# Performance work log

Hardware: AMD Instinct MI355X
Metric: run time of the kernel (lower is better)

## Reference

```python
import jax, jax.numpy as jnp
import numpy as np

EPS = 1e-8      # module eps for attention renorm
LN_EPS = 1e-5   # torch LayerNorm default


def _lin(x, w, b):
    return x @ w + b


def _ln(x, g, b):
    m = jnp.mean(x, -1, keepdims=True)
    v = jnp.var(x, -1, keepdims=True)
    return (x - m) * jax.lax.rsqrt(v + LN_EPS) * g + b


def setup_inputs() -> dict:
    key = jax.random.key(0)
    it = iter(jax.random.split(key, 48))
    B, N, IC, EC, D, S = 8, 32768, 3, 63, 128, 8
    wf = lambda i, o: jax.random.normal(next(it), (i, o), jnp.float32) / np.sqrt(i)
    bf = lambda o: jax.random.normal(next(it), (o,), jnp.float32) * 0.02
    return {
        'inputs': jax.random.normal(next(it), (B, N, IC), jnp.float32),
        'embed_pts': jax.random.normal(next(it), (B, N, EC), jnp.float32),
        'slots_mu': jax.random.normal(next(it), (1, 1, D), jnp.float32),
        'slots_sigma': jax.random.normal(next(it), (1, 1, D), jnp.float32),
        'w0': wf(IC, 64), 'b0': bf(64),
        'w1': wf(64, 32), 'b1': bf(32),
        'w2': wf(32, 32), 'b2': bf(32),
        'w3': wf(32, 32), 'b3': bf(32),
        'w4': wf(32, 32), 'b4': bf(32),
        'w5': wf(32, 32), 'b5': bf(32),
        'w7': wf(IC + EC + 32, D), 'b7': bf(D),
        'wq': wf(D, D), 'bq': bf(D),
        'wk': wf(D, D), 'bk': bf(D),
        'wv': wf(D, D), 'bv': bf(D),
        'ln_in_g': jnp.ones((D,), jnp.float32), 'ln_in_b': jnp.zeros((D,), jnp.float32),
        'ln_sl_g': jnp.ones((D,), jnp.float32), 'ln_sl_b': jnp.zeros((D,), jnp.float32),
        'ln_ff_g': jnp.ones((D,), jnp.float32), 'ln_ff_b': jnp.zeros((D,), jnp.float32),
        'gru_wih': jax.random.normal(next(it), (3 * D, D), jnp.float32) / np.sqrt(D),
        'gru_whh': jax.random.normal(next(it), (3 * D, D), jnp.float32) / np.sqrt(D),
        'gru_bih': bf(3 * D), 'gru_bhh': bf(3 * D),
        'mlp1_w': wf(D, D), 'mlp1_b': bf(D),
        'mlp2_w': wf(D, D), 'mlp2_b': bf(D),
        'num_slots': S,
    }


def reference(inputs, embed_pts, slots_mu, slots_sigma, w0, b0, w1, b1, w2, b2, w3, b3, w4, b4, w5, b5, w7, b7, wq, bq, wk, bk, wv, bv, ln_in_g, ln_in_b, ln_sl_g, ln_sl_b, ln_ff_g, ln_ff_b, gru_wih, gru_whh, gru_bih, gru_bhh, mlp1_w, mlp1_b, mlp2_w, mlp2_b, num_slots):
    # dense stack (no nonlinearities in the original)
    x = inputs
    for w, b in ((w0, b0), (w1, b1), (w2, b2), (w3, b3), (w4, b4), (w5, b5)):
        x = _lin(x, w, b)
    h = _lin(jnp.concatenate([inputs, embed_pts, x], -1), w7, b7)  # [B,N,D]
    B, N, D = h.shape
    scale = D ** -0.5

    # slot init: torch.normal(mean(mu).data, std(sigma).data) over broadcast tensors
    mu = jnp.broadcast_to(slots_mu, (B, num_slots, D))
    sg = jnp.broadcast_to(slots_sigma, (B, num_slots, D))
    mean = jax.lax.stop_gradient(jnp.mean(mu))
    std = jax.lax.stop_gradient(jnp.std(sg, ddof=1))  # torch.std is unbiased
    slots = mean + std * jax.random.normal(jax.random.key(42), (B, num_slots, D), jnp.float32)

    h = _ln(h, ln_in_g, ln_in_b)
    k = _lin(h, wk, bk)
    v = _lin(h, wv, bv)

    for _ in range(3):  # iters
        slots_prev = slots
        q = _lin(_ln(slots, ln_sl_g, ln_sl_b), wq, bq)            # [B,S,D]
        dots = jnp.einsum('bid,bjd->bij', q, k) * scale           # [B,S,N]
        attn = jax.nn.softmax(dots, axis=1) + EPS                 # softmax over slots
        attn = attn / jnp.sum(attn, -1, keepdims=True)            # renorm over inputs
        updates = jnp.einsum('bjd,bij->bid', v, attn)             # [B,S,D]
        # GRUCell (torch semantics)
        xg = updates.reshape(-1, D)
        hp = slots_prev.reshape(-1, D)
        gi = xg @ gru_wih.T + gru_bih                             # [B*S,3D]
        gh = hp @ gru_whh.T + gru_bhh
        ir, iz, inn = jnp.split(gi, 3, axis=-1)
        hr, hz, hn = jnp.split(gh, 3, axis=-1)
        r = jax.nn.sigmoid(ir + hr)
        z = jax.nn.sigmoid(iz + hz)
        n = jnp.tanh(inn + r * hn)
        slots = ((1.0 - z) * n + z * hp).reshape(B, num_slots, D)
        # residual MLP (two linears, no activation, as in source)
        m = _lin(_lin(_ln(slots, ln_ff_g, ln_ff_b), mlp1_w, mlp1_b), mlp2_w, mlp2_b)
        slots = slots + m
    return slots.reshape(B, num_slots * D)
```

## Files before the change

### kernel.cpp

```cpp
#include <hip/hip_runtime.h>


#define B_  8
#define N_  32768
#define NB_ (B_ * N_)
#define D_  128
#define S_  8

typedef unsigned int u32;
typedef unsigned short u16;
typedef __attribute__((ext_vector_type(8))) short bf16x8;
typedef __attribute__((ext_vector_type(4))) float f32x4;

__device__ inline u32 bfr1(float x) {
    u32 u = __float_as_uint(x);
    return (u + 0x7FFFu + ((u >> 16) & 1u)) >> 16;
}
__device__ inline u32 bfpack2(u32 lo, u32 hi) { return lo | (hi << 16); }

__device__ inline void threefry42(u32 c0, u32 c1, u32& o0, u32& o1) {
    const u32 k0 = 0u, k1 = 42u, k2 = 0x1BD11BDAu ^ 0u ^ 42u;
    const u32 ks[3] = {k0, k1, k2};
    u32 x0 = c0 + k0, x1 = c1 + k1;
    const int rA[4] = {13, 15, 26, 6}, rB[4] = {17, 29, 16, 24};
#pragma unroll
    for (int i = 0; i < 5; i++) {
#pragma unroll
        for (int k = 0; k < 4; k++) {
            int r = (i & 1) ? rB[k] : rA[k];
            x0 += x1;
            x1 = (x1 << r) | (x1 >> (32 - r));
            x1 ^= x0;
        }
        x0 += ks[(i + 1) % 3];
        x1 += ks[(i + 2) % 3] + (u32)(i + 1);
    }
    o0 = x0; o1 = x1;
}

__device__ inline float bits_to_normal(u32 b) {
    float f = __uint_as_float((b >> 9) | 0x3f800000u) - 1.0f;
    const float lo = -0.99999994f;
    float r = fmaxf(lo, f * 1.99999994f + lo);
    float w = -log1pf(-r * r);
    float p;
    if (w < 5.0f) {
        w -= 2.5f;
        p = 2.81022636e-08f;
        p = fmaf(p, w, 3.43273939e-07f);
        p = fmaf(p, w, -3.5233877e-06f);
        p = fmaf(p, w, -4.39150654e-06f);
        p = fmaf(p, w, 0.00021858087f);
        p = fmaf(p, w, -0.00125372503f);
        p = fmaf(p, w, -0.00417768164f);
        p = fmaf(p, w, 0.246640727f);
        p = fmaf(p, w, 1.50140941f);
    } else {
        w = sqrtf(w) - 3.0f;
        p = -0.000200214257f;
        p = fmaf(p, w, 0.000100950558f);
        p = fmaf(p, w, 0.00134934322f);
        p = fmaf(p, w, -0.00367342844f);
        p = fmaf(p, w, 0.00573950773f);
        p = fmaf(p, w, -0.0076224613f);
        p = fmaf(p, w, 0.00943887047f);
        p = fmaf(p, w, 1.00167406f);
        p = fmaf(p, w, 2.83297682f);
    }
    return 1.41421356f * (p * r);
}

__device__ inline float block128_sum(float v, float* red) {
#pragma unroll
    for (int o = 32; o; o >>= 1) v += __shfl_down(v, o);
    __syncthreads();
    if ((threadIdx.x & 63) == 0) red[threadIdx.x >> 6] = v;
    __syncthreads();
    return red[0] + red[1];
}

__device__ void emit_q(float x, int bs,
                       const float* lnsg, const float* lnsb,
                       const float* wq, const float* bq,
                       const float* wkT, const float* bk,
                       float* qt, float* qc,
                       float* shA, float* red) {
    int t = threadIdx.x;
    float m = block128_sum(x, red) * (1.0f / 128.0f);
    float e = x - m;
    float var = block128_sum(e * e, red) * (1.0f / 128.0f);
    float inv = rsqrtf(var + 1e-5f);
    __syncthreads();
    shA[t] = fmaf(e * inv, lnsg[t], lnsb[t]);
    __syncthreads();
    float q = bq[t];
#pragma unroll 4
    for (int i = 0; i < 128; i++) q = fmaf(shA[i], wq[i * 128 + t], q);
    __syncthreads();
    shA[t] = q;
    __syncthreads();
    float a2 = 0.f;
#pragma unroll 4
    for (int j = 0; j < 128; j++) a2 = fmaf(wkT[j * 128 + t], shA[j], a2);
    const float scale = 0.08838834764831845f;
    qt[bs * 128 + t] = a2 * scale;
    float pr = block128_sum(shA[t] * bk[t], red);
    if (t == 0) qc[bs] = pr * scale;
}


__global__ __launch_bounds__(256) void k0_transpose(
    const float* __restrict__ wih, const float* __restrict__ whh,
    const float* __restrict__ wk,
    float* __restrict__ wihT, float* __restrict__ whhT, float* __restrict__ wkT) {
    int idx = blockIdx.x * 256 + threadIdx.x;
    if (idx < 49152) {
        int d = idx / 384, g = idx % 384;
        wihT[idx] = wih[g * 128 + d];
    } else if (idx < 98304) {
        int o = idx - 49152;
        int d = o / 384, g = o % 384;
        whhT[o] = whh[g * 128 + d];
    } else if (idx < 114688) {
        int o = idx - 98304;
        int j = o >> 7, tcol = o & 127;
        wkT[o] = wk[tcol * 128 + j];
    }
}


__global__ __launch_bounds__(256) void k1_setup(
    const float* __restrict__ w0, const float* __restrict__ b0,
    const float* __restrict__ w1, const float* __restrict__ b1,
    const float* __restrict__ w2, const float* __restrict__ b2,
    const float* __restrict__ w3, const float* __restrict__ b3,
    const float* __restrict__ w4, const float* __restrict__ b4,
    const float* __restrict__ w5, const float* __restrict__ b5,
    const float* __restrict__ w7, const float* __restrict__ b7,
    const float* __restrict__ mu, const float* __restrict__ sg,
    float* __restrict__ Wh, float* __restrict__ bh, float* __restrict__ slots,
    u16* __restrict__ whiT) {
    __shared__ float A[192], Bt[96], bb[64], bb2[32];
    __shared__ float stats[2];
    int t = threadIdx.x;
    for (int i = t; i < 192; i += 256) A[i] = w0[i];
    for (int i = t; i < 64; i += 256) bb[i] = b0[i];
    __syncthreads();
    const float* wl[5] = {w1, w2, w3, w4, w5};
    const float* bl[5] = {b1, b2, b3, b4, b5};
    int kin = 64;
    for (int l = 0; l < 5; l++) {
        const float* w = wl[l];
        const float* bias = bl[l];
        if (t < 96) {
            int i = t / 32, j = t % 32;
            float acc = 0.f;
            for (int k = 0; k < kin; k++) acc += A[i * kin + k] * w[k * 32 + j];
            Bt[i * 32 + j] = acc;
        } else if (t < 128) {
            int j = t - 96;
            float acc = bias[j];
            for (int k = 0; k < kin; k++) acc += bb[k] * w[k * 32 + j];
            bb2[j] = acc;
        }
        __syncthreads();
        if (t < 96) A[t] = Bt[t];
        if (t < 32) bb[t] = bb2[t];
        __syncthreads();
        kin = 32;
    }
    for (int idx = t; idx < 66 * 128; idx += 256) {
        int i = idx >> 7, j = idx & 127;
        float acc = w7[idx];
        if (i < 3) {
            for (int k = 0; k < 32; k++) acc += A[i * 32 + k] * w7[(66 + k) * 128 + j];
        }
        Wh[idx] = acc;
    }
    for (int j = t; j < 128; j += 256) {
        float acc = b7[j];
        for (int k = 0; k < 32; k++) acc += bb[k] * w7[(66 + k) * 128 + j];
        bh[j] = acc;
    }
    if (t == 0) {
        float s1 = 0.f, s2 = 0.f;
        for (int d = 0; d < 128; d++) { s1 += mu[d]; s2 += sg[d]; }
        float mmu = s1 / 128.f, msg = s2 / 128.f;
        float ss = 0.f;
        for (int d = 0; d < 128; d++) { float e = sg[d] - msg; ss += e * e; }
        stats[0] = mmu;
        stats[1] = sqrtf(64.f * ss / 8191.f);
    }
    __syncthreads();
    for (int idx = t; idx < 128 * 96; idx += 256) {
        int col = idx / 96, k = idx - col * 96;
        float v = (k < 66) ? Wh[k * 128 + col] : 0.f;
        whiT[idx] = (u16)bfr1(v);
    }
    float mean = stats[0], sd = stats[1];
    for (int p = t; p < 8192; p += 256) {
        u32 o0, o1;
        threefry42(0u, (u32)p, o0, o1);
        slots[p] = fmaf(sd, bits_to_normal(o0 ^ o1), mean);
    }
}


__global__ __launch_bounds__(256) void k2_hln(
    const float* __restrict__ inputs, const float* __restrict__ embed,
    const u16* __restrict__ whiT, const float* __restrict__ bh,
    const float* __restrict__ g, const float* __restrict__ bbias,
    u16* __restrict__ hlnb) {
    __shared__ __align__(16) char smem[34816];
    __shared__ float bhl[128], gl[128], bl[128];
    int t = threadIdx.x;
    u16* ebuf = (u16*)smem;
    size_t rbase = (size_t)blockIdx.x * 128;
    for (int idx = t; idx < 384; idx += 256)
        ebuf[(idx / 3) * 104 + (idx % 3)] = (u16)bfr1(inputs[rbase * 3 + idx]);
    for (int idx = t; idx < 128 * 63; idx += 256) {
        int r = idx / 63, i = idx - r * 63;
        ebuf[r * 104 + 3 + i] = (u16)bfr1(embed[rbase * 63 + idx]);
    }
    for (int idx = t; idx < 128 * 30; idx += 256) {
        int r = idx / 30, i = idx - r * 30;
        ebuf[r * 104 + 66 + i] = 0;
    }
    if (t < 128) { bhl[t] = bh[t]; gl[t] = g[t]; bl[t] = bbias[t]; }
    __syncthreads();

    int w = t >> 6, l = t & 63;
    int c16 = l & 15, g4 = l >> 4;
    int wr0 = w * 32;
    float bhc[8], gc[8], bc[8];
#pragma unroll
    for (int nt = 0; nt < 8; nt++) {
        bhc[nt] = bhl[nt * 16 + c16];
        gc[nt] = gl[nt * 16 + c16];
        bc[nt] = bl[nt * 16 + c16];
    }
    f32x4 acc[2][8];
#pragma unroll
    for (int mi = 0; mi < 2; mi++)
#pragma unroll
        for (int nt = 0; nt < 8; nt++)
            acc[mi][nt] = (f32x4){bhc[nt], bhc[nt], bhc[nt], bhc[nt]};

#pragma unroll
    for (int kc = 0; kc < 3; kc++) {
        bf16x8 a0 = *(const bf16x8*)&ebuf[(wr0 + c16) * 104 + kc * 32 + g4 * 8];
        bf16x8 a1 = *(const bf16x8*)&ebuf[(wr0 + 16 + c16) * 104 + kc * 32 + g4 * 8];
#pragma unroll
        for (int nt = 0; nt < 8; nt++) {
            uint4 bw = *(const uint4*)(whiT + (size_t)(nt * 16 + c16) * 96 + kc * 32 + g4 * 8);
            bf16x8 bf = *(bf16x8*)&bw;
            acc[0][nt] = __builtin_amdgcn_mfma_f32_16x16x32_bf16(a0, bf, acc[0][nt], 0, 0, 0);
            acc[1][nt] = __builtin_amdgcn_mfma_f32_16x16x32_bf16(a1, bf, acc[1][nt], 0, 0, 0);
        }
    }

    __syncthreads();
    u16* T = (u16*)smem;
#pragma unroll
    for (int mi = 0; mi < 2; mi++) {
#pragma unroll
        for (int i = 0; i < 4; i++) {
            float s = 0.f;
#pragma unroll
            for (int nt = 0; nt < 8; nt++) s += acc[mi][nt][i];
            s += __shfl_xor(s, 1); s += __shfl_xor(s, 2);
            s += __shfl_xor(s, 4); s += __shfl_xor(s, 8);
            float m = s * (1.0f / 128.0f);
            float v = 0.f;
#pragma unroll
            for (int nt = 0; nt < 8; nt++) { float d = acc[mi][nt][i] - m; v = fmaf(d, d, v); }
            v += __shfl_xor(v, 1); v += __shfl_xor(v, 2);
            v += __shfl_xor(v, 4); v += __shfl_xor(v, 8);
            float inv = rsqrtf(v * (1.0f / 128.0f) + 1e-5f);
            int row = wr0 + mi * 16 + g4 * 4 + i;
#pragma unroll
            for (int nt = 0; nt < 8; nt++) {
                float val = fmaf((acc[mi][nt][i] - m) * inv, gc[nt], bc[nt]);
                T[row * 136 + nt * 16 + c16] = (u16)bfr1(val);
            }
        }
    }
    __syncthreads();
    {
        int r = t >> 1, hf = t & 1;
        const u16* Tr = T + r * 136 + hf * 64;
        u16* dst = hlnb + (rbase + r) * 128 + hf * 64;
#pragma unroll
        for (int j = 0; j < 8; j++) {
            uint4 v = *(const uint4*)(Tr + j * 8);
            *(uint4*)(dst + j * 8) = v;
        }
    }
}


__global__ __launch_bounds__(128) void k3_q(
    const float* __restrict__ slots,
    const float* __restrict__ lnsg, const float* __restrict__ lnsb,
    const float* __restrict__ wq, const float* __restrict__ bq,
    const float* __restrict__ wkT, const float* __restrict__ bk,
    float* __restrict__ qt, float* __restrict__ qc) {
    __shared__ float shA[128];
    __shared__ float red[2];
    int bs = blockIdx.x;
    float x = slots[bs * 128 + threadIdx.x];
    emit_q(x, bs, lnsg, lnsb, wq, bq, wkT, bk, qt, qc, shA, red);
}


__global__ __launch_bounds__(256) void k4_attn(
    const uint4* __restrict__ hlnb4,
    const float* __restrict__ qt, const float* __restrict__ qc,
    float* __restrict__ vecp, float* __restrict__ denp) {
    __shared__ __align__(16) u16 tiles[4][32 * 132];
    __shared__ __align__(16) u16 attnP[4][16 * 40];
    __shared__ __align__(16) float vlds[2][1024];
    __shared__ float dlds[4][8];
    int t = threadIdx.x;
    int w = t >> 6, l = t & 63;
    int blk = blockIdx.x;
    int b = blk >> 8, slab = blk & 255;
    size_t row0 = (size_t)b * N_ + (size_t)slab * 128 + (size_t)w * 32;
    int c16 = l & 15, g = l >> 4;
    u16* tw = tiles[w];

    bf16x8 qf[4];
#pragma unroll
    for (int kc = 0; kc < 4; kc++) {
        uint4 qu = {0u, 0u, 0u, 0u};
        if (c16 < 8) {
            const float* qp = qt + b * 1024 + c16 * 128 + kc * 32 + g * 8;
            float4 qa = *(const float4*)qp;
            float4 qb = *(const float4*)(qp + 4);
            qu.x = bfpack2(bfr1(qa.x), bfr1(qa.y));
            qu.y = bfpack2(bfr1(qa.z), bfr1(qa.w));
            qu.z = bfpack2(bfr1(qb.x), bfr1(qb.y));
            qu.w = bfpack2(bfr1(qb.z), bfr1(qb.w));
        }
        qf[kc] = *(bf16x8*)&qu;
    }
    float qcv = (c16 < 8) ? qc[b * 8 + c16] : 0.f;

    f32x4 dacc[2];
    dacc[0] = (f32x4){0.f, 0.f, 0.f, 0.f};
    dacc[1] = (f32x4){0.f, 0.f, 0.f, 0.f};
#pragma unroll
    for (int mt = 0; mt < 2; mt++) {
#pragma unroll
        for (int kc = 0; kc < 4; kc++) {
            uint4 au = hlnb4[(row0 + mt * 16 + c16) * 16 + kc * 4 + g];
            dacc[mt] = __builtin_amdgcn_mfma_f32_16x16x32_bf16(*(bf16x8*)&au, qf[kc], dacc[mt], 0, 0, 0);
            int off = (mt * 16 + c16) * 132 + kc * 32 + g * 8;
            uint2 lo; lo.x = au.x; lo.y = au.y;
            uint2 hi; hi.x = au.z; hi.y = au.w;
            *(uint2*)&tw[off] = lo;
            *(uint2*)&tw[off + 4] = hi;
        }
    }

    float denacc = 0.f;
#pragma unroll
    for (int mt = 0; mt < 2; mt++) {
        float pv[4];
#pragma unroll
        for (int r = 0; r < 4; r++) {
            float v = dacc[mt][r] + qcv;
            float mx = v;
            mx = fmaxf(mx, __shfl_xor(mx, 1));
            mx = fmaxf(mx, __shfl_xor(mx, 2));
            mx = fmaxf(mx, __shfl_xor(mx, 4));
            float e = __expf(v - mx);
            float ssum = e;
            ssum += __shfl_xor(ssum, 1);
            ssum += __shfl_xor(ssum, 2);
            ssum += __shfl_xor(ssum, 4);
            float a = (c16 < 8) ? fmaf(e, 1.0f / ssum, 1e-8f) : 0.f;
            pv[r] = a;
            denacc += a;
        }
        uint2 pw;
        pw.x = bfpack2(bfr1(pv[0]), bfr1(pv[1]));
        pw.y = bfpack2(bfr1(pv[2]), bfr1(pv[3]));
        *(uint2*)&attnP[w][c16 * 40 + mt * 16 + g * 4] = pw;
    }
    denacc += __shfl_xor(denacc, 16);
    denacc += __shfl_xor(denacc, 32);
    if (l < 8) dlds[w][l] = denacc;

    uint4 afu = *(const uint4*)&attnP[w][c16 * 40 + g * 8];
    bf16x8 af = *(bf16x8*)&afu;
    f32x4 uacc[8];
#pragma unroll
    for (int nt = 0; nt < 8; nt++) uacc[nt] = (f32x4){0.f, 0.f, 0.f, 0.f};
#pragma unroll
    for (int nt = 0; nt < 8; nt++) {
        const u16* tp = tw + nt * 16 + c16;
        u32 w0 = (u32)tp[(g * 8 + 0) * 132] | ((u32)tp[(g * 8 + 1) * 132] << 16);
        u32 w1 = (u32)tp[(g * 8 + 2) * 132] | ((u32)tp[(g * 8 + 3) * 132] << 16);
        u32 w2 = (u32)tp[(g * 8 + 4) * 132] | ((u32)tp[(g * 8 + 5) * 132] << 16);
        u32 w3 = (u32)tp[(g * 8 + 6) * 132] | ((u32)tp[(g * 8 + 7) * 132] << 16);
        uint4 bu; bu.x = w0; bu.y = w1; bu.z = w2; bu.w = w3;
        uacc[nt] = __builtin_amdgcn_mfma_f32_16x16x32_bf16(af, *(bf16x8*)&bu, uacc[nt], 0, 0, 0);
    }
    if (w < 2 && g < 2) {
#pragma unroll
        for (int nt = 0; nt < 8; nt++)
#pragma unroll
            for (int r = 0; r < 4; r++)
                vlds[w][(g * 4 + r) * 128 + nt * 16 + c16] = uacc[nt][r];
    }
    __syncthreads();
    if (w >= 2 && g < 2) {
#pragma unroll
        for (int nt = 0; nt < 8; nt++)
#pragma unroll
            for (int r = 0; r < 4; r++)
                vlds[w - 2][(g * 4 + r) * 128 + nt * 16 + c16] += uacc[nt][r];
    }
    __syncthreads();
    float* vout = vecp + ((size_t)blk << 10);
#pragma unroll
    for (int rep = 0; rep < 4; rep++) {
        int o = rep * 256 + t;
        vout[o] = vlds[0][o] + vlds[1][o];
    }
    if (t < 8) denp[blk * 8 + t] = dlds[0][t] + dlds[1][t] + dlds[2][t] + dlds[3][t];
}


__device__ inline float sum512(float v, float* red8) {
#pragma unroll
    for (int o = 32; o; o >>= 1) v += __shfl_down(v, o);
    __syncthreads();
    if ((threadIdx.x & 63) == 0) red8[threadIdx.x >> 6] = v;
    __syncthreads();
    float s = 0.f;
#pragma unroll
    for (int i = 0; i < 8; i++) s += red8[i];
    return s;
}

__device__ inline float reduce4(float part, float* praw, int qq, int d) {
    __syncthreads();
    praw[qq * 128 + d] = part;
    __syncthreads();
    return praw[d] + praw[128 + d] + praw[256 + d] + praw[384 + d];
}

__global__ __launch_bounds__(512) void k5_update(
    const float* __restrict__ vecp, const float* __restrict__ denp,
    const float* __restrict__ wv, const float* __restrict__ bv,
    const float* __restrict__ wihT, const float* __restrict__ whhT,
    const float* __restrict__ bih, const float* __restrict__ bhh,
    const float* __restrict__ lnfg, const float* __restrict__ lnfb,
    const float* __restrict__ m1w, const float* __restrict__ m1b,
    const float* __restrict__ m2w, const float* __restrict__ m2b,
    float* __restrict__ slots,
    const float* __restrict__ lnsg, const float* __restrict__ lnsb,
    const float* __restrict__ wq, const float* __restrict__ bq,
    const float* __restrict__ wkT, const float* __restrict__ bk,
    float* __restrict__ qt, float* __restrict__ qc,
    float* __restrict__ out, int compute_q, int write_out) {
    __shared__ float sA[128], sB[128], sC[128], sH[128], sQ[128];
    __shared__ float praw[512];
    __shared__ float red8[8];
    __shared__ float gsc[6][512];
    int t = threadIdx.x;
    int bs = blockIdx.x;
    int b = bs >> 3, slot = bs & 7;
    int d = t & 127, qq = t >> 7;

    float dvp = (t < 256) ? denp[((size_t)(b * 256) + t) * 8 + slot] : 0.f;
    float dv = sum512(dvp, red8);

    float vs = 0.f;
    const float* vp0 = vecp + (((size_t)(b * 256 + qq * 64)) << 10) + slot * 128 + d;
#pragma unroll 8
    for (int s = 0; s < 64; s++) vs += vp0[(size_t)s << 10];
    float vtot = reduce4(vs, praw, qq, d);
    if (qq == 0) { sA[d] = vtot / dv; sC[d] = slots[bs * 128 + d]; }
    __syncthreads();

    float up = 0.f;
    {
        const float* wvp = wv + (size_t)(qq * 32) * 128 + d;
#pragma unroll 8
        for (int i = 0; i < 32; i++) up = fmaf(sA[qq * 32 + i], wvp[i * 128], up);
    }
    float updt = reduce4(up, praw, qq, d) + bv[d];
    if (qq == 0) sB[d] = updt;
    __syncthreads();

#pragma unroll 1
    for (int gx = 0; gx < 3; gx++) {
        int g = gx * 128 + d;
        float ap = 0.f, hp = 0.f;
        const float* wi = wihT + (size_t)(qq * 32) * 384 + g;
        const float* wh = whhT + (size_t)(qq * 32) * 384 + g;
#pragma unroll 8
        for (int i = 0; i < 32; i++) {
            ap = fmaf(sB[qq * 32 + i], wi[i * 384], ap);
            hp = fmaf(sC[qq * 32 + i], wh[i * 384], hp);
        }
        gsc[gx * 2][t] = ap;
        gsc[gx * 2 + 1][t] = hp;
    }
    __syncthreads();
    float gi0 = gsc[0][d] + gsc[0][128 + d] + gsc[0][256 + d] + gsc[0][384 + d] + bih[d];
    float gh0 = gsc[1][d] + gsc[1][128 + d] + gsc[1][256 + d] + gsc[1][384 + d] + bhh[d];
    float gi1 = gsc[2][d] + gsc[2][128 + d] + gsc[2][256 + d] + gsc[2][384 + d] + bih[128 + d];
    float gh1 = gsc[3][d] + gsc[3][128 + d] + gsc[3][256 + d] + gsc[3][384 + d] + bhh[128 + d];
    float gi2 = gsc[4][d] + gsc[4][128 + d] + gsc[4][256 + d] + gsc[4][384 + d] + bih[256 + d];
    float gh2 = gsc[5][d] + gsc[5][128 + d] + gsc[5][256 + d] + gsc[5][384 + d] + bhh[256 + d];
    float rg = 1.f / (1.f + expf(-(gi0 + gh0)));
    float zg = 1.f / (1.f + expf(-(gi1 + gh1)));
    float ng = tanhf(fmaf(rg, gh2, gi2));
    float hnew = (1.f - zg) * ng + zg * sC[d];
    __syncthreads();
    if (qq == 0) sH[d] = hnew;
    __syncthreads();

    float xh = (t < 128) ? sH[t] : 0.f;
    float mh = sum512(xh, red8) * (1.0f / 128.0f);
    float eh = xh - mh;
    float vh = sum512((t < 128) ? eh * eh : 0.f, red8) * (1.0f / 128.0f);
    float invh = rsqrtf(vh + 1e-5f);
    __syncthreads();
    if (t < 128) sA[t] = fmaf(eh * invh, lnfg[t], lnfb[t]);
    __syncthreads();

    float p1 = 0.f;
    {
        const float* m1p = m1w + (size_t)(qq * 32) * 128 + d;
#pragma unroll 8
        for (int i = 0; i < 32; i++) p1 = fmaf(sA[qq * 32 + i], m1p[i * 128], p1);
    }
    float m1v = reduce4(p1, praw, qq, d) + m1b[d];
    if (qq == 0) sB[d] = m1v;
    __syncthreads();

    float p2 = 0.f;
    {
        const float* m2p = m2w + (size_t)(qq * 32) * 128 + d;
#pragma unroll 8
        for (int i = 0; i < 32; i++) p2 = fmaf(sB[qq * 32 + i], m2p[i * 128], p2);
    }
    float m2v = reduce4(p2, praw, qq, d) + m2b[d];
    float snew = sH[d] + m2v;
    __syncthreads();
    if (qq == 0) {
        slots[bs * 128 + d] = snew;
        if (write_out) out[bs * 128 + d] = snew;
        sH[d] = snew;
    }
    __syncthreads();

    if (compute_q) {
        float xs = (t < 128) ? sH[t] : 0.f;
        float ms = sum512(xs, red8) * (1.0f / 128.0f);
        float es = xs - ms;
        float vs2 = sum512((t < 128) ? es * es : 0.f, red8) * (1.0f / 128.0f);
        float invs = rsqrtf(vs2 + 1e-5f);
        __syncthreads();
        if (t < 128) sA[t] = fmaf(es * invs, lnsg[t], lnsb[t]);
        __syncthreads();
        float pq = 0.f;
        {
            const float* wqp = wq + (size_t)(qq * 32) * 128 + d;
#pragma unroll 8
            for (int i = 0; i < 32; i++) pq = fmaf(sA[qq * 32 + i], wqp[i * 128], pq);
        }
        float qv = reduce4(pq, praw, qq, d) + bq[d];
        if (qq == 0) sQ[d] = qv;
        __syncthreads();
        float pa = 0.f;
        {
            const float* wkp = wkT + (size_t)(qq * 32) * 128 + d;
#pragma unroll 8
            for (int j = 0; j < 32; j++) pa = fmaf(wkp[j * 128], sQ[qq * 32 + j], pa);
        }
        const float scale = 0.08838834764831845f;
        float a2 = reduce4(pa, praw, qq, d) * scale;
        if (qq == 0) qt[bs * 128 + d] = a2;
        float xpr = (t < 128) ? sQ[t] * bk[t] : 0.f;
        float pr = sum512(xpr, red8);
        if (t == 0) qc[bs] = pr * scale;
    }
}


extern "C" void kernel_launch(void* const* d_in, const int* in_sizes, int n_in,
                              void* d_out, int out_size, void* d_ws, size_t ws_size,
                              hipStream_t stream) {
    const float* inputs = (const float*)d_in[0];
    const float* embed  = (const float*)d_in[1];
    const float* mu     = (const float*)d_in[2];
    const float* sg     = (const float*)d_in[3];
    const float* w0 = (const float*)d_in[4];  const float* b0 = (const float*)d_in[5];
    const float* w1 = (const float*)d_in[6];  const float* b1 = (const float*)d_in[7];
    const float* w2 = (const float*)d_in[8];  const float* b2 = (const float*)d_in[9];
    const float* w3 = (const float*)d_in[10]; const float* b3 = (const float*)d_in[11];
    const float* w4 = (const float*)d_in[12]; const float* b4 = (const float*)d_in[13];
    const float* w5 = (const float*)d_in[14]; const float* b5 = (const float*)d_in[15];
    const float* w7 = (const float*)d_in[16]; const float* b7 = (const float*)d_in[17];
    const float* wq = (const float*)d_in[18]; const float* bq = (const float*)d_in[19];
    const float* wk = (const float*)d_in[20]; const float* bk = (const float*)d_in[21];
    const float* wv = (const float*)d_in[22]; const float* bv = (const float*)d_in[23];
    const float* ln_in_g = (const float*)d_in[24]; const float* ln_in_b = (const float*)d_in[25];
    const float* ln_sl_g = (const float*)d_in[26]; const float* ln_sl_b = (const float*)d_in[27];
    const float* ln_ff_g = (const float*)d_in[28]; const float* ln_ff_b = (const float*)d_in[29];
    const float* gwih = (const float*)d_in[30]; const float* gwhh = (const float*)d_in[31];
    const float* gbih = (const float*)d_in[32]; const float* gbhh = (const float*)d_in[33];
    const float* m1w = (const float*)d_in[34]; const float* m1b = (const float*)d_in[35];
    const float* m2w = (const float*)d_in[36]; const float* m2b = (const float*)d_in[37];

    char* ws = (char*)d_ws;
    u16* hlnb = (u16*)ws;
    size_t off = (size_t)NB_ * 128 * 2;
    float* Wh    = (float*)(ws + off); off += 66 * 128 * 4;
    float* bh    = (float*)(ws + off); off += 128 * 4;
    float* slots = (float*)(ws + off); off += 64 * 128 * 4;
    float* qt    = (float*)(ws + off); off += 64 * 128 * 4;
    float* qc    = (float*)(ws + off); off += 64 * 4;
    float* vecp  = (float*)(ws + off); off += (size_t)2048 * 1024 * 4;
    float* denp  = (float*)(ws + off); off += 2048 * 8 * 4;
    float* wihT  = (float*)(ws + off); off += 384 * 128 * 4;
    float* whhT  = (float*)(ws + off); off += 384 * 128 * 4;
    float* wkT   = (float*)(ws + off); off += 128 * 128 * 4;
    u16* whiT    = (u16*)(ws + off); off += 128 * 96 * 2;

    k0_transpose<<<448, 256, 0, stream>>>(gwih, gwhh, wk, wihT, whhT, wkT);
    k1_setup<<<1, 256, 0, stream>>>(w0, b0, w1, b1, w2, b2, w3, b3, w4, b4, w5, b5,
                                    w7, b7, mu, sg, Wh, bh, slots, whiT);
    k2_hln<<<NB_ / 128, 256, 0, stream>>>(inputs, embed, whiT, bh,
                                          ln_in_g, ln_in_b, hlnb);
    k3_q<<<64, 128, 0, stream>>>(slots, ln_sl_g, ln_sl_b, wq, bq, wkT, bk, qt, qc);
    for (int it = 0; it < 3; it++) {
        k4_attn<<<2048, 256, 0, stream>>>((const uint4*)hlnb, qt, qc, vecp, denp);
        k5_update<<<64, 512, 0, stream>>>(vecp, denp, wv, bv, wihT, whhT, gbih, gbhh,
                                          ln_ff_g, ln_ff_b, m1w, m1b, m2w, m2b, slots,
                                          ln_sl_g, ln_sl_b, wq, bq, wkT, bk, qt, qc,
                                          (float*)d_out, (it < 2) ? 1 : 0, (it == 2) ? 1 : 0);
    }
}
```

Baseline: 273.9 us.

## Process two row tiles per attention block with register prefetch and transposed LDS tile

Each attention block now covers 256 rows instead of 128, so the grid is halved. Each wave handles two 32-row sub-tiles in sequence, and it loads the second tile into registers while the first tile's softmax and update MFMAs run. The staged tile is stored transposed in LDS (row-contiguous per feature), so the update MFMA operand becomes two vector reads instead of eight scalar gathers, at the cost of scattered 16-bit LDS writes. The vector accumulation buffer now reuses the tile LDS. The update kernel reduces half as many partials, which shrinks the vecp/denp traffic and workspace.

Result: faster. 261.9 us (-4.4%).

```diff
diff --git a/kernel.cpp b/kernel.cpp
--- a/kernel.cpp
+++ b/kernel.cpp
@@ -317,15 +317,14 @@
     const uint4* __restrict__ hlnb4,
     const float* __restrict__ qt, const float* __restrict__ qc,
     float* __restrict__ vecp, float* __restrict__ denp) {
-    __shared__ __align__(16) u16 tiles[4][32 * 132];
+    __shared__ __align__(16) u16 tiles[4][128 * 36];
     __shared__ __align__(16) u16 attnP[4][16 * 40];
-    __shared__ __align__(16) float vlds[2][1024];
     __shared__ float dlds[4][8];
     int t = threadIdx.x;
     int w = t >> 6, l = t & 63;
     int blk = blockIdx.x;
-    int b = blk >> 8, slab = blk & 255;
-    size_t row0 = (size_t)b * N_ + (size_t)slab * 128 + (size_t)w * 32;
+    int b = blk >> 7, slab = blk & 127;
+    size_t row0 = (size_t)b * N_ + (size_t)slab * 256 + (size_t)w * 32;
     int c16 = l & 15, g = l >> 4;
     u16* tw = tiles[w];
 
@@ -346,88 +345,113 @@
     }
     float qcv = (c16 < 8) ? qc[b * 8 + c16] : 0.f;
 
-    f32x4 dacc[2];
-    dacc[0] = (f32x4){0.f, 0.f, 0.f, 0.f};
-    dacc[1] = (f32x4){0.f, 0.f, 0.f, 0.f};
-#pragma unroll
-    for (int mt = 0; mt < 2; mt++) {
-#pragma unroll
-        for (int kc = 0; kc < 4; kc++) {
-            uint4 au = hlnb4[(row0 + mt * 16 + c16) * 16 + kc * 4 + g];
-            dacc[mt] = __builtin_amdgcn_mfma_f32_16x16x32_bf16(*(bf16x8*)&au, qf[kc], dacc[mt], 0, 0, 0);
-            int off = (mt * 16 + c16) * 132 + kc * 32 + g * 8;
-            uint2 lo; lo.x = au.x; lo.y = au.y;
-            uint2 hi; hi.x = au.z; hi.y = au.w;
-            *(uint2*)&tw[off] = lo;
-            *(uint2*)&tw[off + 4] = hi;
-        }
-    }
-
+    f32x4 uacc[8];
+#pragma unroll
+    for (int nt = 0; nt < 8; nt++) uacc[nt] = (f32x4){0.f, 0.f, 0.f, 0.f};
     float denacc = 0.f;
-#pragma unroll
-    for (int mt = 0; mt < 2; mt++) {
-        float pv[4];
-#pragma unroll
-        for (int r = 0; r < 4; r++) {
-            float v = dacc[mt][r] + qcv;
-            float mx = v;
-            mx = fmaxf(mx, __shfl_xor(mx, 1));
-            mx = fmaxf(mx, __shfl_xor(mx, 2));
-            mx = fmaxf(mx, __shfl_xor(mx, 4));
-            float e = __expf(v - mx);
-            float ssum = e;
-            ssum += __shfl_xor(ssum, 1);
-            ssum += __shfl_xor(ssum, 2);
-            ssum += __shfl_xor(ssum, 4);
-            float a = (c16 < 8) ? fmaf(e, 1.0f / ssum, 1e-8f) : 0.f;
-            pv[r] = a;
-            denacc += a;
-        }
-        uint2 pw;
-        pw.x = bfpack2(bfr1(pv[0]), bfr1(pv[1]));
-        pw.y = bfpack2(bfr1(pv[2]), bfr1(pv[3]));
-        *(uint2*)&attnP[w][c16 * 40 + mt * 16 + g * 4] = pw;
+
+    uint4 st[8];
+#pragma unroll
+    for (int mt = 0; mt < 2; mt++)
+#pragma unroll
+        for (int kc = 0; kc < 4; kc++)
+            st[mt * 4 + kc] = hlnb4[(row0 + mt * 16 + c16) * 16 + kc * 4 + g];
+
+    for (int tt = 0; tt < 2; tt++) {
+        f32x4 dacc[2];
+        dacc[0] = (f32x4){0.f, 0.f, 0.f, 0.f};
+        dacc[1] = (f32x4){0.f, 0.f, 0.f, 0.f};
+#pragma unroll
+        for (int mt = 0; mt < 2; mt++) {
+#pragma unroll
+            for (int kc = 0; kc < 4; kc++) {
+                uint4 au = st[mt * 4 + kc];
+                dacc[mt] = __builtin_amdgcn_mfma_f32_16x16x32_bf16(*(bf16x8*)&au, qf[kc], dacc[mt], 0, 0, 0);
+                int r = mt * 16 + c16;
+                int d0 = kc * 32 + g * 8;
+                tw[(d0 + 0) * 36 + r] = (u16)(au.x & 0xFFFF);
+                tw[(d0 + 1) * 36 + r] = (u16)(au.x >> 16);
+                tw[(d0 + 2) * 36 + r] = (u16)(au.y & 0xFFFF);
+                tw[(d0 + 3) * 36 + r] = (u16)(au.y >> 16);
+                tw[(d0 + 4) * 36 + r] = (u16)(au.z & 0xFFFF);
+                tw[(d0 + 5) * 36 + r] = (u16)(au.z >> 16);
+                tw[(d0 + 6) * 36 + r] = (u16)(au.w & 0xFFFF);
+                tw[(d0 + 7) * 36 + r] = (u16)(au.w >> 16);
+            }
+        }
+        if (tt == 0) {
+            size_t rowB = row0 + 128;
+#pragma unroll
+            for (int mt = 0; mt < 2; mt++)
+#pragma unroll
+                for (int kc = 0; kc < 4; kc++)
+                    st[mt * 4 + kc] = hlnb4[(rowB + mt * 16 + c16) * 16 + kc * 4 + g];
+        }
+#pragma unroll
+        for (int mt = 0; mt < 2; mt++) {
+            float pv[4];
+#pragma unroll
+            for (int r = 0; r < 4; r++) {
+                float v = dacc[mt][r] + qcv;
+                float mx = v;
+                mx = fmaxf(mx, __shfl_xor(mx, 1));
+                mx = fmaxf(mx, __shfl_xor(mx, 2));
+                mx = fmaxf(mx, __shfl_xor(mx, 4));
+                float e = __expf(v - mx);
+                float ssum = e;
+                ssum += __shfl_xor(ssum, 1);
+                ssum += __shfl_xor(ssum, 2);
+                ssum += __shfl_xor(ssum, 4);
+                float a = (c16 < 8) ? fmaf(e, 1.0f / ssum, 1e-8f) : 0.f;
+                pv[r] = a;
+                denacc += a;
+            }
+            uint2 pw;
+            pw.x = bfpack2(bfr1(pv[0]), bfr1(pv[1]));
+            pw.y = bfpack2(bfr1(pv[2]), bfr1(pv[3]));
+            *(uint2*)&attnP[w][c16 * 40 + mt * 16 + g * 4] = pw;
+        }
+        uint4 afu = *(const uint4*)&attnP[w][c16 * 40 + g * 8];
+        bf16x8 af = *(bf16x8*)&afu;
+#pragma unroll
+        for (int nt = 0; nt < 8; nt++) {
+            const u16* tp = tw + (nt * 16 + c16) * 36 + g * 8;
+            uint2 blo = *(const uint2*)tp;
+            uint2 bhi = *(const uint2*)(tp + 4);
+            uint4 bu; bu.x = blo.x; bu.y = blo.y; bu.z = bhi.x; bu.w = bhi.y;
+            uacc[nt] = __builtin_amdgcn_mfma_f32_16x16x32_bf16(af, *(bf16x8*)&bu, uacc[nt], 0, 0, 0);
+        }
     }
     denacc += __shfl_xor(denacc, 16);
     denacc += __shfl_xor(denacc, 32);
     if (l < 8) dlds[w][l] = denacc;
 
-    uint4 afu = *(const uint4*)&attnP[w][c16 * 40 + g * 8];
-    bf16x8 af = *(bf16x8*)&afu;
-    f32x4 uacc[8];
-#pragma unroll
-    for (int nt = 0; nt < 8; nt++) uacc[nt] = (f32x4){0.f, 0.f, 0.f, 0.f};
-#pragma unroll
-    for (int nt = 0; nt < 8; nt++) {
-        const u16* tp = tw + nt * 16 + c16;
-        u32 w0 = (u32)tp[(g * 8 + 0) * 132] | ((u32)tp[(g * 8 + 1) * 132] << 16);
-        u32 w1 = (u32)tp[(g * 8 + 2) * 132] | ((u32)tp[(g * 8 + 3) * 132] << 16);
-        u32 w2 = (u32)tp[(g * 8 + 4) * 132] | ((u32)tp[(g * 8 + 5) * 132] << 16);
-        u32 w3 = (u32)tp[(g * 8 + 6) * 132] | ((u32)tp[(g * 8 + 7) * 132] << 16);
-        uint4 bu; bu.x = w0; bu.y = w1; bu.z = w2; bu.w = w3;
-        uacc[nt] = __builtin_amdgcn_mfma_f32_16x16x32_bf16(af, *(bf16x8*)&bu, uacc[nt], 0, 0, 0);
-    }
+    __syncthreads();
+    float* vlds0 = (float*)&tiles[0][0];
+    float* vlds1 = vlds0 + 1024;
     if (w < 2 && g < 2) {
+        float* vb = (w == 0) ? vlds0 : vlds1;
 #pragma unroll
         for (int nt = 0; nt < 8; nt++)
 #pragma unroll
             for (int r = 0; r < 4; r++)
-                vlds[w][(g * 4 + r) * 128 + nt * 16 + c16] = uacc[nt][r];
+                vb[(g * 4 + r) * 128 + nt * 16 + c16] = uacc[nt][r];
     }
     __syncthreads();
     if (w >= 2 && g < 2) {
+        float* vb = (w == 2) ? vlds0 : vlds1;
 #pragma unroll
         for (int nt = 0; nt < 8; nt++)
 #pragma unroll
             for (int r = 0; r < 4; r++)
-                vlds[w - 2][(g * 4 + r) * 128 + nt * 16 + c16] += uacc[nt][r];
+                vb[(g * 4 + r) * 128 + nt * 16 + c16] += uacc[nt][r];
     }
     __syncthreads();
     float* vout = vecp + ((size_t)blk << 10);
 #pragma unroll
     for (int rep = 0; rep < 4; rep++) {
         int o = rep * 256 + t;
-        vout[o] = vlds[0][o] + vlds[1][o];
+        vout[o] = vlds0[o] + vlds1[o];
     }
     if (t < 8) denp[blk * 8 + t] = dlds[0][t] + dlds[1][t] + dlds[2][t] + dlds[3][t];
 }
@@ -475,13 +499,13 @@
     int b = bs >> 3, slot = bs & 7;
     int d = t & 127, qq = t >> 7;
 
-    float dvp = (t < 256) ? denp[((size_t)(b * 256) + t) * 8 + slot] : 0.f;
+    float dvp = (t < 128) ? denp[((size_t)(b * 128) + t) * 8 + slot] : 0.f;
     float dv = sum512(dvp, red8);
 
     float vs = 0.f;
-    const float* vp0 = vecp + (((size_t)(b * 256 + qq * 64)) << 10) + slot * 128 + d;
+    const float* vp0 = vecp + (((size_t)(b * 128 + qq * 32)) << 10) + slot * 128 + d;
 #pragma unroll 8
-    for (int s = 0; s < 64; s++) vs += vp0[(size_t)s << 10];
+    for (int s = 0; s < 32; s++) vs += vp0[(size_t)s << 10];
     float vtot = reduce4(vs, praw, qq, d);
     if (qq == 0) { sA[d] = vtot / dv; sC[d] = slots[bs * 128 + d]; }
     __syncthreads();
@@ -627,8 +651,8 @@
     float* slots = (float*)(ws + off); off += 64 * 128 * 4;
     float* qt    = (float*)(ws + off); off += 64 * 128 * 4;
     float* qc    = (float*)(ws + off); off += 64 * 4;
-    float* vecp  = (float*)(ws + off); off += (size_t)2048 * 1024 * 4;
-    float* denp  = (float*)(ws + off); off += 2048 * 8 * 4;
+    float* vecp  = (float*)(ws + off); off += (size_t)1024 * 1024 * 4;
+    float* denp  = (float*)(ws + off); off += 1024 * 8 * 4;
     float* wihT  = (float*)(ws + off); off += 384 * 128 * 4;
     float* whhT  = (float*)(ws + off); off += 384 * 128 * 4;
     float* wkT   = (float*)(ws + off); off += 128 * 128 * 4;
@@ -641,7 +665,7 @@
                                           ln_in_g, ln_in_b, hlnb);
     k3_q<<<64, 128, 0, stream>>>(slots, ln_sl_g, ln_sl_b, wq, bq, wkT, bk, qt, qc);
     for (int it = 0; it < 3; it++) {
-        k4_attn<<<2048, 256, 0, stream>>>((const uint4*)hlnb, qt, qc, vecp, denp);
+        k4_attn<<<1024, 256, 0, stream>>>((const uint4*)hlnb, qt, qc, vecp, denp);
         k5_update<<<64, 512, 0, stream>>>(vecp, denp, wv, bv, wihT, whhT, gbih, gbhh,
                                           ln_ff_g, ln_ff_b, m1w, m1b, m2w, m2b, slots,
                                           ln_sl_g, ln_sl_b, wq, bq, wkT, bk, qt, qc,
```
